# Kernel tuning notes

Measured on AMD Instinct MI355X. Metric: run time of the kernel, lower is better.

The kernel has to match this reference:

```python
import jax, jax.numpy as jnp
import numpy as np


def setup_inputs() -> dict:
    key = jax.random.key(0)
    n_class, n_support, n_query, feature_dim = 32, 16, 16, 1024
    n_rows = n_class * n_support + n_query * n_class  # 1024
    data = jax.random.normal(key, (n_rows, feature_dim), dtype=jnp.float32)
    return {"data": data, "n_class": n_class, "n_support": n_support, "n_query": n_query}


def reference(data, n_class, n_support, n_query):
    D = data.shape[-1]
    # support: [n_class, n_support, D]; query: [n_query*n_class, D]
    support = data[: n_class * n_support].reshape(n_class, n_support, D)
    query = data[n_class * n_support :]
    # attention score: tanh(elementwise product) summed over feature dim
    # scores: [Q, n_class, n_support]  (Q = n_query*n_class)
    scores = jnp.tanh(support[None, :, :, :] * query[:, None, None, :]).sum(-1)
    att = jax.nn.softmax(scores, axis=-1)  # softmax over n_support
    # weighted instance pooling -> prototypes per (query, class): [Q, n_class, D]
    proto = jnp.einsum("qcs,csd->qcd", att, support)
    return proto
```

## Files before the change

### kernel.cpp

```cpp
#include <hip/hip_runtime.h>

constexpr int NC = 32, NS = 16, NQ = 512, D = 1024;
constexpr int QPB = 8;
constexpr int F4H = 128;

__device__ __forceinline__ float pair_term(float t0, float t1) {
    t0 = fminf(t0, 60.f);
    t1 = fminf(t1, 60.f);
    float x = __builtin_amdgcn_exp2f(t0) + 1.f;
    float y = __builtin_amdgcn_exp2f(t1) + 1.f;
    return (x + y) * __builtin_amdgcn_rcpf(x * y);
}

__global__ __launch_bounds__(256, 2)
void proto_attn_kernel(const float* __restrict__ data, float* __restrict__ out) {
    const int c    = blockIdx.x;
    const int qt   = blockIdx.y;
    const int tid  = threadIdx.x;
    const int wave = tid >> 6;
    const int lane = tid & 63;

    __shared__ float4 sup4[NS * F4H];

    const float4* sg = reinterpret_cast<const float4*>(data + (size_t)c * NS * D);

    const float K = 2.88539008177792681472f;
    const int q0 = qt * QPB + wave * 2;
    const float4* qg0 = reinterpret_cast<const float4*>(data + (size_t)(NC * NS + q0) * D);
    const float4* qg1 = qg0 + 256;
    float4 qa[4], qb[4];
    #pragma unroll
    for (int j = 0; j < 4; ++j) {
        float4 t0 = qg0[lane + 64 * j];
        float4 t1 = qg1[lane + 64 * j];
        qa[j] = make_float4(t0.x * K, t0.y * K, t0.z * K, t0.w * K);
        qb[j] = make_float4(t1.x * K, t1.y * K, t1.z * K, t1.w * K);
    }

    #pragma unroll
    for (int i = 0; i < 8; ++i) {
        int idx = tid + 256 * i;
        sup4[idx] = sg[((idx >> 7) << 8) + (idx & 127)];
    }
    __syncthreads();

    float sc0[NS], sc1[NS];
    #pragma unroll
    for (int s = 0; s < NS; ++s) {
        float u0 = 0.f, v0 = 0.f, u1 = 0.f, v1 = 0.f;
        #pragma unroll
        for (int jj = 0; jj < 2; ++jj) {
            float4 sv = sup4[s * F4H + lane + 64 * jj];
            float4 qA = qa[jj], qB = qb[jj];
            u0 += pair_term(sv.x * qA.x, sv.y * qA.y);
            v0 += pair_term(sv.z * qA.z, sv.w * qA.w);
            u1 += pair_term(sv.x * qB.x, sv.y * qB.y);
            v1 += pair_term(sv.z * qB.z, sv.w * qB.w);
        }
        sc0[s] = u0 + v0;
        sc1[s] = u1 + v1;
    }
    __syncthreads();

    #pragma unroll
    for (int i = 0; i < 8; ++i) {
        int idx = tid + 256 * i;
        sup4[idx] = sg[((idx >> 7) << 8) + 128 + (idx & 127)];
    }
    __syncthreads();

    #pragma unroll
    for (int s = 0; s < NS; ++s) {
        float u0 = 0.f, v0 = 0.f, u1 = 0.f, v1 = 0.f;
        #pragma unroll
        for (int jj = 0; jj < 2; ++jj) {
            float4 sv = sup4[s * F4H + lane + 64 * jj];
            float4 qA = qa[2 + jj], qB = qb[2 + jj];
            u0 += pair_term(sv.x * qA.x, sv.y * qA.y);
            v0 += pair_term(sv.z * qA.z, sv.w * qA.w);
            u1 += pair_term(sv.x * qB.x, sv.y * qB.y);
            v1 += pair_term(sv.z * qB.z, sv.w * qB.w);
        }
        sc0[s] += u0 + v0;
        sc1[s] += u1 + v1;
    }

    #pragma unroll
    for (int s = 0; s < NS; ++s) {
        float r0 = sc0[s], r1 = sc1[s];
        #pragma unroll
        for (int m = 32; m >= 1; m >>= 1) {
            r0 += __shfl_xor(r0, m, 64);
            r1 += __shfl_xor(r1, m, 64);
        }
        sc0[s] = (float)D - 2.f * r0;
        sc1[s] = (float)D - 2.f * r1;
    }

    const float L2E = 1.44269504088896340736f;
    float m0 = sc0[0], m1 = sc1[0];
    #pragma unroll
    for (int s = 1; s < NS; ++s) { m0 = fmaxf(m0, sc0[s]); m1 = fmaxf(m1, sc1[s]); }
    float sum0 = 0.f, sum1 = 0.f;
    #pragma unroll
    for (int s = 0; s < NS; ++s) {
        sc0[s] = __builtin_amdgcn_exp2f((sc0[s] - m0) * L2E);
        sc1[s] = __builtin_amdgcn_exp2f((sc1[s] - m1) * L2E);
        sum0 += sc0[s];
        sum1 += sc1[s];
    }
    const float inv0 = __builtin_amdgcn_rcpf(sum0);
    const float inv1 = __builtin_amdgcn_rcpf(sum1);
    #pragma unroll
    for (int s = 0; s < NS; ++s) { sc0[s] *= inv0; sc1[s] *= inv1; }

    float* orow0 = out + ((size_t)q0 * NC + c) * D;
    float* orow1 = orow0 + (size_t)NC * D;

    {
        float4 o0[2], o1[2];
        o0[0] = o0[1] = o1[0] = o1[1] = make_float4(0.f, 0.f, 0.f, 0.f);
        #pragma unroll
        for (int s = 0; s < NS; ++s) {
            const float a0 = sc0[s], a1 = sc1[s];
            #pragma unroll
            for (int jj = 0; jj < 2; ++jj) {
                float4 sv = sup4[s * F4H + lane + 64 * jj];
                o0[jj].x += a0 * sv.x; o0[jj].y += a0 * sv.y;
                o0[jj].z += a0 * sv.z; o0[jj].w += a0 * sv.w;
                o1[jj].x += a1 * sv.x; o1[jj].y += a1 * sv.y;
                o1[jj].z += a1 * sv.z; o1[jj].w += a1 * sv.w;
            }
        }
        float4* og0 = reinterpret_cast<float4*>(orow0) + 128;
        float4* og1 = reinterpret_cast<float4*>(orow1) + 128;
        #pragma unroll
        for (int jj = 0; jj < 2; ++jj) {
            og0[lane + 64 * jj] = o0[jj];
            og1[lane + 64 * jj] = o1[jj];
        }
    }
    __syncthreads();

    #pragma unroll
    for (int i = 0; i < 8; ++i) {
        int idx = tid + 256 * i;
        sup4[idx] = sg[((idx >> 7) << 8) + (idx & 127)];
    }
    __syncthreads();
    {
        float4 o0[2], o1[2];
        o0[0] = o0[1] = o1[0] = o1[1] = make_float4(0.f, 0.f, 0.f, 0.f);
        #pragma unroll
        for (int s = 0; s < NS; ++s) {
            const float a0 = sc0[s], a1 = sc1[s];
            #pragma unroll
            for (int jj = 0; jj < 2; ++jj) {
                float4 sv = sup4[s * F4H + lane + 64 * jj];
                o0[jj].x += a0 * sv.x; o0[jj].y += a0 * sv.y;
                o0[jj].z += a0 * sv.z; o0[jj].w += a0 * sv.w;
                o1[jj].x += a1 * sv.x; o1[jj].y += a1 * sv.y;
                o1[jj].z += a1 * sv.z; o1[jj].w += a1 * sv.w;
            }
        }
        float4* og0 = reinterpret_cast<float4*>(orow0);
        float4* og1 = reinterpret_cast<float4*>(orow1);
        #pragma unroll
        for (int jj = 0; jj < 2; ++jj) {
            og0[lane + 64 * jj] = o0[jj];
            og1[lane + 64 * jj] = o1[jj];
        }
    }
}

extern "C" void kernel_launch(void* const* d_in, const int* in_sizes, int n_in,
                              void* d_out, int out_size, void* d_ws, size_t ws_size,
                              hipStream_t stream) {
    (void)in_sizes; (void)n_in; (void)out_size; (void)d_ws; (void)ws_size;
    const float* data = (const float*)d_in[0];
    float* out = (float*)d_out;
    dim3 grid(NC, NQ / QPB);
    proto_attn_kernel<<<grid, dim3(256), 0, stream>>>(data, out);
}
```

Measured before the change: 143.3 us.

## Prefetch support halves into registers during compute and use nontemporal output stores

Each support half is now loaded from global memory into registers while the previous half is being processed, then copied into LDS after a barrier. This overlaps global-load latency with the tanh score computation and the weighted sum. Query loads are split so only half are held at a time, which frees registers for the prefetch buffer. Output stores become nontemporal, and the fminf clamp in the tanh term is removed; the clamp could matter for large products, though exp2 overflowing to inf still gives a correct limit.

```diff
diff --git a/kernel.cpp b/kernel.cpp
--- a/kernel.cpp
+++ b/kernel.cpp
@@ -4,9 +4,9 @@
 constexpr int QPB = 8;
 constexpr int F4H = 128;
 
+typedef float v4f __attribute__((ext_vector_type(4)));
+
 __device__ __forceinline__ float pair_term(float t0, float t1) {
-    t0 = fminf(t0, 60.f);
-    t1 = fminf(t1, 60.f);
     float x = __builtin_amdgcn_exp2f(t0) + 1.f;
     float y = __builtin_amdgcn_exp2f(t1) + 1.f;
     return (x + y) * __builtin_amdgcn_rcpf(x * y);
@@ -23,26 +23,35 @@
     __shared__ float4 sup4[NS * F4H];
 
     const float4* sg = reinterpret_cast<const float4*>(data + (size_t)c * NS * D);
-
     const float K = 2.88539008177792681472f;
     const int q0 = qt * QPB + wave * 2;
     const float4* qg0 = reinterpret_cast<const float4*>(data + (size_t)(NC * NS + q0) * D);
     const float4* qg1 = qg0 + 256;
-    float4 qa[4], qb[4];
+
+    float4 pre[8];
     #pragma unroll
-    for (int j = 0; j < 4; ++j) {
+    for (int i = 0; i < 8; ++i) {
+        int idx = tid + 256 * i;
+        pre[i] = sg[((idx >> 7) << 8) + (idx & 127)];
+    }
+    #pragma unroll
+    for (int i = 0; i < 8; ++i) sup4[tid + 256 * i] = pre[i];
+    __syncthreads();
+
+    #pragma unroll
+    for (int i = 0; i < 8; ++i) {
+        int idx = tid + 256 * i;
+        pre[i] = sg[((idx >> 7) << 8) + 128 + (idx & 127)];
+    }
+
+    float4 qa[2], qb[2];
+    #pragma unroll
+    for (int j = 0; j < 2; ++j) {
         float4 t0 = qg0[lane + 64 * j];
         float4 t1 = qg1[lane + 64 * j];
         qa[j] = make_float4(t0.x * K, t0.y * K, t0.z * K, t0.w * K);
         qb[j] = make_float4(t1.x * K, t1.y * K, t1.z * K, t1.w * K);
     }
-
-    #pragma unroll
-    for (int i = 0; i < 8; ++i) {
-        int idx = tid + 256 * i;
-        sup4[idx] = sg[((idx >> 7) << 8) + (idx & 127)];
-    }
-    __syncthreads();
 
     float sc0[NS], sc1[NS];
     #pragma unroll
@@ -51,11 +60,10 @@
         #pragma unroll
         for (int jj = 0; jj < 2; ++jj) {
             float4 sv = sup4[s * F4H + lane + 64 * jj];
-            float4 qA = qa[jj], qB = qb[jj];
-            u0 += pair_term(sv.x * qA.x, sv.y * qA.y);
-            v0 += pair_term(sv.z * qA.z, sv.w * qA.w);
-            u1 += pair_term(sv.x * qB.x, sv.y * qB.y);
-            v1 += pair_term(sv.z * qB.z, sv.w * qB.w);
+            u0 += pair_term(sv.x * qa[jj].x, sv.y * qa[jj].y);
+            v0 += pair_term(sv.z * qa[jj].z, sv.w * qa[jj].w);
+            u1 += pair_term(sv.x * qb[jj].x, sv.y * qb[jj].y);
+            v1 += pair_term(sv.z * qb[jj].z, sv.w * qb[jj].w);
         }
         sc0[s] = u0 + v0;
         sc1[s] = u1 + v1;
@@ -63,11 +71,16 @@
     __syncthreads();
 
     #pragma unroll
-    for (int i = 0; i < 8; ++i) {
-        int idx = tid + 256 * i;
-        sup4[idx] = sg[((idx >> 7) << 8) + 128 + (idx & 127)];
+    for (int i = 0; i < 8; ++i) sup4[tid + 256 * i] = pre[i];
+    __syncthreads();
+
+    #pragma unroll
+    for (int j = 0; j < 2; ++j) {
+        float4 t0 = qg0[lane + 64 * (2 + j)];
+        float4 t1 = qg1[lane + 64 * (2 + j)];
+        qa[j] = make_float4(t0.x * K, t0.y * K, t0.z * K, t0.w * K);
+        qb[j] = make_float4(t1.x * K, t1.y * K, t1.z * K, t1.w * K);
     }
-    __syncthreads();
 
     #pragma unroll
     for (int s = 0; s < NS; ++s) {
@@ -75,14 +88,19 @@
         #pragma unroll
         for (int jj = 0; jj < 2; ++jj) {
             float4 sv = sup4[s * F4H + lane + 64 * jj];
-            float4 qA = qa[2 + jj], qB = qb[2 + jj];
-            u0 += pair_term(sv.x * qA.x, sv.y * qA.y);
-            v0 += pair_term(sv.z * qA.z, sv.w * qA.w);
-            u1 += pair_term(sv.x * qB.x, sv.y * qB.y);
-            v1 += pair_term(sv.z * qB.z, sv.w * qB.w);
+            u0 += pair_term(sv.x * qa[jj].x, sv.y * qa[jj].y);
+            v0 += pair_term(sv.z * qa[jj].z, sv.w * qa[jj].w);
+            u1 += pair_term(sv.x * qb[jj].x, sv.y * qb[jj].y);
+            v1 += pair_term(sv.z * qb[jj].z, sv.w * qb[jj].w);
         }
         sc0[s] += u0 + v0;
         sc1[s] += u1 + v1;
+    }
+
+    #pragma unroll
+    for (int i = 0; i < 8; ++i) {
+        int idx = tid + 256 * i;
+        pre[i] = sg[((idx >> 7) << 8) + (idx & 127)];
     }
 
     #pragma unroll
@@ -132,21 +150,18 @@
                 o1[jj].z += a1 * sv.z; o1[jj].w += a1 * sv.w;
             }
         }
-        float4* og0 = reinterpret_cast<float4*>(orow0) + 128;
-        float4* og1 = reinterpret_cast<float4*>(orow1) + 128;
+        v4f* og0 = reinterpret_cast<v4f*>(orow0) + 128;
+        v4f* og1 = reinterpret_cast<v4f*>(orow1) + 128;
         #pragma unroll
         for (int jj = 0; jj < 2; ++jj) {
-            og0[lane + 64 * jj] = o0[jj];
-            og1[lane + 64 * jj] = o1[jj];
+            __builtin_nontemporal_store(*reinterpret_cast<v4f*>(&o0[jj]), og0 + lane + 64 * jj);
+            __builtin_nontemporal_store(*reinterpret_cast<v4f*>(&o1[jj]), og1 + lane + 64 * jj);
         }
     }
     __syncthreads();
 
     #pragma unroll
-    for (int i = 0; i < 8; ++i) {
-        int idx = tid + 256 * i;
-        sup4[idx] = sg[((idx >> 7) << 8) + (idx & 127)];
-    }
+    for (int i = 0; i < 8; ++i) sup4[tid + 256 * i] = pre[i];
     __syncthreads();
     {
         float4 o0[2], o1[2];
@@ -163,12 +178,12 @@
                 o1[jj].z += a1 * sv.z; o1[jj].w += a1 * sv.w;
             }
         }
-        float4* og0 = reinterpret_cast<float4*>(orow0);
-        float4* og1 = reinterpret_cast<float4*>(orow1);
+        v4f* og0 = reinterpret_cast<v4f*>(orow0);
+        v4f* og1 = reinterpret_cast<v4f*>(orow1);
         #pragma unroll
         for (int jj = 0; jj < 2; ++jj) {
-            og0[lane + 64 * jj] = o0[jj];
-            og1[lane + 64 * jj] = o1[jj];
+            __builtin_nontemporal_store(*reinterpret_cast<v4f*>(&o0[jj]), og0 + lane + 64 * jj);
+            __builtin_nontemporal_store(*reinterpret_cast<v4f*>(&o1[jj]), og1 + lane + 64 * jj);
         }
     }
 }
```

New measurement: 155.6 us. 8.6% more time.
